# Kernel tuning notes

Hardware: AMD Instinct MI355X
Metric: run time of the kernel (lower is better)

## Reference

```python
import jax, jax.numpy as jnp
import numpy as np

NUM_HEADS = 12


def setup_inputs() -> dict:
    key = jax.random.key(0)
    k0, k1, k2 = jax.random.split(key, 3)
    B, S, D = 2, 2048, 1536
    scale = 1.0 / np.sqrt(D)
    return {
        "hidden_states": jax.random.normal(k0, (B, S, D), dtype=jnp.float32),
        "W_fc": jax.random.normal(k1, (D, D), dtype=jnp.float32) * scale,
        "b_fc": jnp.zeros((D,), dtype=jnp.float32),
        "W_proj": jax.random.normal(k2, (D, D), dtype=jnp.float32) * scale,
        "b_proj": jnp.zeros((D,), dtype=jnp.float32),
    }


def reference(hidden_states, W_fc, b_fc, W_proj, b_proj):
    B, S, D = hidden_states.shape
    H = NUM_HEADS
    hd = D // H
    # value_states: [B, H, S, hd] (key_states == value_states in the original)
    v = (hidden_states @ W_fc.T + b_fc).reshape(B, S, H, hd).transpose(0, 2, 1, 3)
    # Uniform-weight causal sliding-window attention, window_h = 2^(h+1)-1.
    i = jnp.arange(S)[:, None]          # query pos
    j = jnp.arange(S)[None, :]          # key pos
    w = (2 ** jnp.arange(1, H + 1, dtype=jnp.int32) - 1)[:, None, None]  # [H,1,1]
    mask = (j <= i) & (j >= i - w + 1)                                    # [H,S,S]
    valid_len = jnp.minimum(i + 1, w).astype(v.dtype)                     # [H,S,1]
    attn = jnp.where(mask, 1.0 / valid_len, 0.0)                          # [H,S,S]
    # [H,S,S] x [B,H,S,hd] -> [B,S,H,hd] -> [B,S,D]
    out = jnp.einsum("hqk,bhkd->bqhd", attn, v).reshape(B, S, D)
    attn_weights = jnp.broadcast_to(attn[None], (B, H, S, S))
    return out @ W_proj.T + b_proj, attn_weights
```

## Files before the change

### kernel.cpp

```cpp
#include <hip/hip_runtime.h>
#include <hip/hip_bf16.h>

#define S_LEN   2048
#define DMODEL  1536
#define NBATCH  2
#define NHEADS  12
#define MROWS   (NBATCH * S_LEN)
#define NCHUNK  64

#define NGEMM_BLK  384
#define AWB        640
#define AW_ROWS_PER_B  24576u

#define CVT_BLK    10752
#define WA_BLK     3072

typedef unsigned short u16;
typedef __attribute__((ext_vector_type(8))) short bf16x8;
typedef __attribute__((ext_vector_type(4))) float f32x4;

__device__ __forceinline__ u16 f2bf(float x) {
  unsigned u = __float_as_uint(x);
  u += 0x7fffu + ((u >> 16) & 1u);
  return (u16)(u >> 16);
}
__device__ __forceinline__ float bf2f(u16 x) {
  return __uint_as_float(((unsigned)x) << 16);
}

__device__ __forceinline__ void aw_band(float* __restrict__ aw, unsigned r0,
                                        unsigned rcnt, unsigned wv, unsigned nwv) {
  const int lane = threadIdx.x & 63;
  for (unsigned r = r0 + wv; r < r0 + rcnt; r += nwv) {
    const int i  = (int)(r & (S_LEN - 1u));
    const int bh = (int)(r >> 11);
    const int h  = bh >= NHEADS ? bh - NHEADS : bh;
    const int w  = (2 << h) - 1;
    const int lo = max(0, i - w + 1);
    const int len = i - lo + 1;
    const float inv = 1.0f / (float)len;
    float* p = aw + ((size_t)bh << 22) + ((size_t)i << 11) + lo;

    const int mis  = (int)(((size_t)p >> 2) & 3u);
    const int head = min(len, (4 - mis) & 3);
    if (lane < head) p[lane] = inv;
    const int rem = len - head;
    float* pb = p + head;
    const int nv = rem >> 2;
    const f32x4 rv = {inv, inv, inv, inv};
    for (int k = lane; k < nv; k += 64)
      __builtin_nontemporal_store(rv, &((f32x4*)pb)[k]);
    const int tail = rem & 3;
    if (lane < tail) pb[(nv << 2) + lane] = inv;
  }
}

#define N4_HID  1572864
#define N4_W    589824
__global__ void cvt_all(const float4* __restrict__ h, const float4* __restrict__ wf,
                        const float4* __restrict__ wp, ushort4* __restrict__ ho,
                        ushort4* __restrict__ wfo, ushort4* __restrict__ wpo) {
  int t = blockIdx.x * blockDim.x + threadIdx.x;
  const float4* src;
  ushort4* dst;
  int idx;
  if (t < N4_HID)            { src = h;  dst = ho;  idx = t; }
  else if (t < N4_HID + N4_W){ src = wf; dst = wfo; idx = t - N4_HID; }
  else                       { src = wp; dst = wpo; idx = t - N4_HID - N4_W; }
  float4 f = src[idx];
  ushort4 o;
  o.x = f2bf(f.x); o.y = f2bf(f.y); o.z = f2bf(f.z); o.w = f2bf(f.w);
  dst[idx] = o;
}

__device__ __forceinline__ void gld_lds16(u16* lds, const u16* g) {
  __builtin_amdgcn_global_load_lds(
      (const __attribute__((address_space(1))) unsigned int*)g,
      (__attribute__((address_space(3))) unsigned int*)lds, 16, 0, 0);
}

template <bool WITH_CSUM, typename CT>
__global__ __launch_bounds__(256)
void gemm_aw(const u16* __restrict__ A, const u16* __restrict__ B,
             const float* __restrict__ bias, CT* __restrict__ C,
             float* __restrict__ cs, float* __restrict__ aw,
             unsigned row0, int Ndim, int Kdim) {
  if ((int)blockIdx.x >= NGEMM_BLK) {
    const unsigned wv = (blockIdx.x - NGEMM_BLK) * 4u + ((threadIdx.x >> 6) & 3u);
    aw_band(aw, row0, AW_ROWS_PER_B, wv, AWB * 4u);
    return;
  }

  __shared__ __align__(16) u16 As[2][128 * 32];
  __shared__ __align__(16) u16 Bs[2][128 * 32];
  __shared__ float colpart[4][128];

  const int tid  = threadIdx.x;
  const int wave = tid >> 6;
  const int lane = tid & 63;
  const int l15  = lane & 15;
  const int quad = lane >> 4;
  const int bm = (blockIdx.x / (DMODEL / 128)) * 128;
  const int bn = (blockIdx.x % (DMODEL / 128)) * 128;
  const int wm = (wave >> 1) * 64;
  const int wn = (wave & 1) * 64;

  f32x4 acc[4][4] = {};

  const int srow = wave * 32 + (lane >> 2);
  const int skk  = (lane & 3) * 8;
  const u16* gA = A + (size_t)(bm + srow) * Kdim + skk;
  const u16* gB = B + (size_t)(bn + srow) * Kdim + skk;
  u16* lA = (u16*)&As[0][(wave * 32) * 32] - (size_t)0;
  const int lofs = (wave * 32) * 32;
  const size_t rstep16 = (size_t)16 * Kdim;

  gld_lds16(&As[0][lofs],           gA);
  gld_lds16(&As[0][lofs + 16 * 32], gA + rstep16);
  gld_lds16(&Bs[0][lofs],           gB);
  gld_lds16(&Bs[0][lofs + 16 * 32], gB + rstep16);

  int cur = 0;
  for (int k0 = 0; k0 < Kdim; k0 += 32) {
    __syncthreads();
    if (k0 + 32 < Kdim) {
      const int nxt = cur ^ 1;
      gld_lds16(&As[nxt][lofs],           gA + k0 + 32);
      gld_lds16(&As[nxt][lofs + 16 * 32], gA + k0 + 32 + rstep16);
      gld_lds16(&Bs[nxt][lofs],           gB + k0 + 32);
      gld_lds16(&Bs[nxt][lofs + 16 * 32], gB + k0 + 32 + rstep16);
    }

    bf16x8 af[4], bfr[4];
#pragma unroll
    for (int i = 0; i < 4; ++i)
      af[i] = *(const bf16x8*)&As[cur][(wm + i * 16 + l15) * 32 + quad * 8];
#pragma unroll
    for (int j = 0; j < 4; ++j)
      bfr[j] = *(const bf16x8*)&Bs[cur][(wn + j * 16 + l15) * 32 + quad * 8];
#pragma unroll
    for (int i = 0; i < 4; ++i)
#pragma unroll
      for (int j = 0; j < 4; ++j)
        acc[i][j] = __builtin_amdgcn_mfma_f32_16x16x32_bf16(af[i], bfr[j], acc[i][j], 0, 0, 0);
    cur ^= 1;
  }

  const int r0 = quad * 4;
#pragma unroll
  for (int j = 0; j < 4; ++j) {
    const int col = bn + wn + j * 16 + l15;
    const float bj = bias[col];
    float sA = 0.f, sB = 0.f;
#pragma unroll
    for (int i = 0; i < 4; ++i) {
      const int row = bm + wm + i * 16 + r0;
#pragma unroll
      for (int r = 0; r < 4; ++r) {
        float cv = acc[i][j][r] + bj;
        if constexpr (sizeof(CT) == 2) {
          C[(size_t)(row + r) * Ndim + col] = (CT)f2bf(cv);
        } else {
          __builtin_nontemporal_store((CT)cv, &C[(size_t)(row + r) * Ndim + col]);
        }
        if (WITH_CSUM) { if (i < 2) sA += cv; else sB += cv; }
      }
    }
    if (WITH_CSUM) {
      sA += __shfl_xor(sA, 16); sA += __shfl_xor(sA, 32);
      sB += __shfl_xor(sB, 16); sB += __shfl_xor(sB, 32);
      if (quad == 0) {
        colpart[(wm >> 5) | 0][wn + j * 16 + l15] = sA;
        colpart[(wm >> 5) | 1][wn + j * 16 + l15] = sB;
      }
    }
  }
  if (WITH_CSUM) {
    __syncthreads();
    if (tid < 128) {
      const int b  = bm >> 11;
      const int c0 = (bm & 2047) >> 5;
#pragma unroll
      for (int g = 0; g < 4; ++g)
        cs[((size_t)b * NCHUNK + c0 + g) * DMODEL + bn + tid] = colpart[g][tid];
    }
  }
}

__global__ void winavg(const u16* __restrict__ v, const float* __restrict__ cs,
                       u16* __restrict__ A2) {
  int t = blockIdx.x * blockDim.x + threadIdx.x;
  int d = t % DMODEL;
  int s = (t / DMODEL) & 255;
  int b = t / (DMODEL * 256);
  const int h = d >> 7;
  const int w = (2 << h) - 1;
  const u16* vb  = v + (size_t)b * S_LEN * DMODEL + d;
  const float* cb = cs + (size_t)b * NCHUNK * DMODEL + d;

  const int i0 = s * 8;
  const int clead = i0 >> 5;

  int jf = 0, ct = 0;
  const bool ht = (i0 + 7 >= w);
  if (ht) { jf = max(i0, w) - w; ct = jf > 0 ? (jf - 1) >> 5 : 0; }

  float lead = 0.f, tb = 0.f;
  for (int cc = 0; cc < clead; ++cc) {
    float x = cb[(size_t)cc * DMODEL];
    lead += x;
    if (cc < ct) tb += x;
  }
  for (int r = clead * 32; r < i0; ++r)
    lead += bf2f(vb[(size_t)r * DMODEL]);

  float trail = 0.f;
  if (ht && jf > 0) {
    trail = tb;
    for (int r = ct * 32; r < jf; ++r)
      trail += bf2f(vb[(size_t)r * DMODEL]);
  }

  u16* out = A2 + ((size_t)(b * S_LEN + i0)) * DMODEL + d;
#pragma unroll
  for (int rr = 0; rr < 8; ++rr) {
    const int i = i0 + rr;
    lead += bf2f(vb[(size_t)i * DMODEL]);
    float o;
    if (i < w) {
      o = lead / (float)(i + 1);
    } else {
      trail += bf2f(vb[(size_t)(i - w) * DMODEL]);
      o = (lead - trail) / (float)w;
    }
    out[(size_t)rr * DMODEL] = f2bf(o);
  }
}

extern "C" void kernel_launch(void* const* d_in, const int* in_sizes, int n_in,
                              void* d_out, int out_size, void* d_ws, size_t ws_size,
                              hipStream_t stream) {
  const float* hidden = (const float*)d_in[0];
  const float* W_fc   = (const float*)d_in[1];
  const float* b_fc   = (const float*)d_in[2];
  const float* W_proj = (const float*)d_in[3];
  const float* b_proj = (const float*)d_in[4];
  float* outp = (float*)d_out;
  float* aw = outp + (size_t)MROWS * DMODEL;

  char* ws = (char*)d_ws;
  u16*   A16   = (u16*)(ws);
  u16*   Wfc16 = (u16*)(ws + 12582912);
  u16*   Wpj16 = (u16*)(ws + 17301504);
  u16*   v16   = (u16*)(ws + 22020096);
  float* csums = (float*)(ws + 34603008);

  cvt_all<<<CVT_BLK, 256, 0, stream>>>((const float4*)hidden, (const float4*)W_fc,
                                       (const float4*)W_proj, (ushort4*)A16,
                                       (ushort4*)Wfc16, (ushort4*)Wpj16);

  gemm_aw<true, u16><<<NGEMM_BLK + AWB, 256, 0, stream>>>(
      A16, Wfc16, b_fc, v16, csums, aw, 0u, DMODEL, DMODEL);

  winavg<<<WA_BLK, 256, 0, stream>>>(v16, csums, A16);

  gemm_aw<false, float><<<NGEMM_BLK + AWB, 256, 0, stream>>>(
      A16, Wpj16, b_proj, outp, nullptr, aw, AW_ROWS_PER_B, DMODEL, DMODEL);
}
```

Baseline: 519.0 us.

## Fuse fp32-to-bf16 conversion into first GEMM and rebalance attention-weight fill

Removes the standalone conversion kernel. The first GEMM now loads fp32 hidden states and W_fc straight from global memory, converts them to bf16 in registers and stores them to LDS through a register-staged double buffer. W_proj conversion and half of the attention-weight band fill ride along as extra blocks in the first GEMM. The other half of the band fill moves into the window-average kernel, so the second GEMM runs alone. This saves one launch plus a full bf16 round trip of the activations, but the first GEMM now reads twice the bytes and gives up the async global-to-LDS loads.

```diff
diff --git a/kernel.cpp b/kernel.cpp
--- a/kernel.cpp
+++ b/kernel.cpp
@@ -9,11 +9,16 @@
 #define NCHUNK  64
 
 #define NGEMM_BLK  384
-#define AWB        640
+#define WCVT_BLK   256
+#define BAND1_BLK  384
+#define G1_GRID    (NGEMM_BLK + WCVT_BLK + BAND1_BLK)
+
+#define WA_BLK     3072
+#define BAND2_BLK  512
+#define WA_GRID    (WA_BLK + BAND2_BLK)
+
 #define AW_ROWS_PER_B  24576u
-
-#define CVT_BLK    10752
-#define WA_BLK     3072
+#define N4_W    589824u
 
 typedef unsigned short u16;
 typedef __attribute__((ext_vector_type(8))) short bf16x8;
@@ -26,6 +31,10 @@
 }
 __device__ __forceinline__ float bf2f(u16 x) {
   return __uint_as_float(((unsigned)x) << 16);
+}
+__device__ __forceinline__ u16 cvt1(float x) {
+  __hip_bfloat16 h = __float2bfloat16(x);
+  return *(u16*)&h;
 }
 
 __device__ __forceinline__ void aw_band(float* __restrict__ aw, unsigned r0,
@@ -55,45 +64,203 @@
   }
 }
 
-#define N4_HID  1572864
-#define N4_W    589824
-__global__ void cvt_all(const float4* __restrict__ h, const float4* __restrict__ wf,
-                        const float4* __restrict__ wp, ushort4* __restrict__ ho,
-                        ushort4* __restrict__ wfo, ushort4* __restrict__ wpo) {
-  int t = blockIdx.x * blockDim.x + threadIdx.x;
-  const float4* src;
-  ushort4* dst;
-  int idx;
-  if (t < N4_HID)            { src = h;  dst = ho;  idx = t; }
-  else if (t < N4_HID + N4_W){ src = wf; dst = wfo; idx = t - N4_HID; }
-  else                       { src = wp; dst = wpo; idx = t - N4_HID - N4_W; }
-  float4 f = src[idx];
-  ushort4 o;
-  o.x = f2bf(f.x); o.y = f2bf(f.y); o.z = f2bf(f.z); o.w = f2bf(f.w);
-  dst[idx] = o;
-}
-
 __device__ __forceinline__ void gld_lds16(u16* lds, const u16* g) {
   __builtin_amdgcn_global_load_lds(
       (const __attribute__((address_space(1))) unsigned int*)g,
       (__attribute__((address_space(3))) unsigned int*)lds, 16, 0, 0);
 }
 
-template <bool WITH_CSUM, typename CT>
+__device__ __forceinline__ void st8(u16* dst, float4 lo, float4 hi) {
+  ushort4 p0 = { cvt1(lo.x), cvt1(lo.y), cvt1(lo.z), cvt1(lo.w) };
+  ushort4 p1 = { cvt1(hi.x), cvt1(hi.y), cvt1(hi.z), cvt1(hi.w) };
+  *((ushort4*)dst)       = p0;
+  *((ushort4*)(dst + 4)) = p1;
+}
+
 __global__ __launch_bounds__(256)
-void gemm_aw(const u16* __restrict__ A, const u16* __restrict__ B,
-             const float* __restrict__ bias, CT* __restrict__ C,
-             float* __restrict__ cs, float* __restrict__ aw,
-             unsigned row0, int Ndim, int Kdim) {
-  if ((int)blockIdx.x >= NGEMM_BLK) {
-    const unsigned wv = (blockIdx.x - NGEMM_BLK) * 4u + ((threadIdx.x >> 6) & 3u);
-    aw_band(aw, row0, AW_ROWS_PER_B, wv, AWB * 4u);
+void gemm1_fused(const float* __restrict__ A, const float* __restrict__ Bsrc,
+                 const float* __restrict__ bias, u16* __restrict__ C,
+                 float* __restrict__ cs, float* __restrict__ aw,
+                 const float4* __restrict__ wp, ushort4* __restrict__ wpo) {
+  const int blk = blockIdx.x;
+  if (blk >= NGEMM_BLK) {
+    if (blk < NGEMM_BLK + WCVT_BLK) {
+      for (unsigned t = (unsigned)(blk - NGEMM_BLK) * 256u + threadIdx.x;
+           t < N4_W; t += WCVT_BLK * 256u) {
+        float4 f = wp[t];
+        ushort4 o = { f2bf(f.x), f2bf(f.y), f2bf(f.z), f2bf(f.w) };
+        wpo[t] = o;
+      }
+    } else {
+      const unsigned wv = (unsigned)(blk - NGEMM_BLK - WCVT_BLK) * 4u +
+                          ((threadIdx.x >> 6) & 3u);
+      aw_band(aw, 0u, AW_ROWS_PER_B, wv, BAND1_BLK * 4u);
+    }
     return;
   }
 
   __shared__ __align__(16) u16 As[2][128 * 32];
   __shared__ __align__(16) u16 Bs[2][128 * 32];
   __shared__ float colpart[4][128];
+
+  const int tid  = threadIdx.x;
+  const int wave = tid >> 6;
+  const int lane = tid & 63;
+  const int l15  = lane & 15;
+  const int quad = lane >> 4;
+  const int bm = (blk / (DMODEL / 128)) * 128;
+  const int bn = (blk % (DMODEL / 128)) * 128;
+  const int wm = (wave >> 1) * 64;
+  const int wn = (wave & 1) * 64;
+
+  f32x4 acc[4][4] = {};
+
+  const int srow = wave * 32 + (lane >> 2);
+  const int skk  = (lane & 3) * 8;
+  const float* gA = A    + (size_t)(bm + srow) * DMODEL + skk;
+  const float* gB = Bsrc + (size_t)(bn + srow) * DMODEL + skk;
+  const size_t rs16 = (size_t)16 * DMODEL;
+
+  float4 ra0, ra1, ra2, ra3, rb0, rb1, rb2, rb3;
+#define LOADF(k0)                                                        \
+  do {                                                                   \
+    ra0 = *(const float4*)(gA + (k0));                                   \
+    ra1 = *(const float4*)(gA + (k0) + 4);                               \
+    ra2 = *(const float4*)(gA + rs16 + (k0));                            \
+    ra3 = *(const float4*)(gA + rs16 + (k0) + 4);                        \
+    rb0 = *(const float4*)(gB + (k0));                                   \
+    rb1 = *(const float4*)(gB + (k0) + 4);                               \
+    rb2 = *(const float4*)(gB + rs16 + (k0));                            \
+    rb3 = *(const float4*)(gB + rs16 + (k0) + 4);                        \
+  } while (0)
+#define STOREF(buf)                                                      \
+  do {                                                                   \
+    st8(&As[buf][srow * 32 + skk],        ra0, ra1);                     \
+    st8(&As[buf][(srow + 16) * 32 + skk], ra2, ra3);                     \
+    st8(&Bs[buf][srow * 32 + skk],        rb0, rb1);                     \
+    st8(&Bs[buf][(srow + 16) * 32 + skk], rb2, rb3);                     \
+  } while (0)
+
+  LOADF(0);
+  STOREF(0);
+
+  int cur = 0;
+  for (int k0 = 0; k0 < DMODEL; k0 += 32) {
+    __syncthreads();
+    if (k0 + 32 < DMODEL) LOADF(k0 + 32);
+
+    bf16x8 af[4], bfr[4];
+#pragma unroll
+    for (int i = 0; i < 4; ++i)
+      af[i] = *(const bf16x8*)&As[cur][(wm + i * 16 + l15) * 32 + quad * 8];
+#pragma unroll
+    for (int j = 0; j < 4; ++j)
+      bfr[j] = *(const bf16x8*)&Bs[cur][(wn + j * 16 + l15) * 32 + quad * 8];
+#pragma unroll
+    for (int i = 0; i < 4; ++i)
+#pragma unroll
+      for (int j = 0; j < 4; ++j)
+        acc[i][j] = __builtin_amdgcn_mfma_f32_16x16x32_bf16(af[i], bfr[j], acc[i][j], 0, 0, 0);
+
+    if (k0 + 32 < DMODEL) STOREF(cur ^ 1);
+    cur ^= 1;
+  }
+#undef LOADF
+#undef STOREF
+
+  const int r0 = quad * 4;
+#pragma unroll
+  for (int j = 0; j < 4; ++j) {
+    const int col = bn + wn + j * 16 + l15;
+    const float bj = bias[col];
+    float sA = 0.f, sB = 0.f;
+#pragma unroll
+    for (int i = 0; i < 4; ++i) {
+      const int row = bm + wm + i * 16 + r0;
+#pragma unroll
+      for (int r = 0; r < 4; ++r) {
+        float cv = acc[i][j][r] + bj;
+        C[(size_t)(row + r) * DMODEL + col] = f2bf(cv);
+        if (i < 2) sA += cv; else sB += cv;
+      }
+    }
+    sA += __shfl_xor(sA, 16); sA += __shfl_xor(sA, 32);
+    sB += __shfl_xor(sB, 16); sB += __shfl_xor(sB, 32);
+    if (quad == 0) {
+      colpart[(wm >> 5) | 0][wn + j * 16 + l15] = sA;
+      colpart[(wm >> 5) | 1][wn + j * 16 + l15] = sB;
+    }
+  }
+  __syncthreads();
+  if (tid < 128) {
+    const int b  = bm >> 11;
+    const int c0 = (bm & 2047) >> 5;
+#pragma unroll
+    for (int g = 0; g < 4; ++g)
+      cs[((size_t)b * NCHUNK + c0 + g) * DMODEL + bn + tid] = colpart[g][tid];
+  }
+}
+
+__global__ void winavg_aw(const u16* __restrict__ v, const float* __restrict__ cs,
+                          u16* __restrict__ A2, float* __restrict__ aw) {
+  if ((int)blockIdx.x >= WA_BLK) {
+    const unsigned wv = (blockIdx.x - WA_BLK) * 4u + ((threadIdx.x >> 6) & 3u);
+    aw_band(aw, AW_ROWS_PER_B, AW_ROWS_PER_B, wv, BAND2_BLK * 4u);
+    return;
+  }
+  int t = blockIdx.x * blockDim.x + threadIdx.x;
+  int d = t % DMODEL;
+  int s = (t / DMODEL) & 255;
+  int b = t / (DMODEL * 256);
+  const int h = d >> 7;
+  const int w = (2 << h) - 1;
+  const u16* vb  = v + (size_t)b * S_LEN * DMODEL + d;
+  const float* cb = cs + (size_t)b * NCHUNK * DMODEL + d;
+
+  const int i0 = s * 8;
+  const int clead = i0 >> 5;
+
+  int jf = 0, ct = 0;
+  const bool ht = (i0 + 7 >= w);
+  if (ht) { jf = max(i0, w) - w; ct = jf > 0 ? (jf - 1) >> 5 : 0; }
+
+  float lead = 0.f, tb = 0.f;
+  for (int cc = 0; cc < clead; ++cc) {
+    float x = cb[(size_t)cc * DMODEL];
+    lead += x;
+    if (cc < ct) tb += x;
+  }
+  for (int r = clead * 32; r < i0; ++r)
+    lead += bf2f(vb[(size_t)r * DMODEL]);
+
+  float trail = 0.f;
+  if (ht && jf > 0) {
+    trail = tb;
+    for (int r = ct * 32; r < jf; ++r)
+      trail += bf2f(vb[(size_t)r * DMODEL]);
+  }
+
+  u16* out = A2 + ((size_t)(b * S_LEN + i0)) * DMODEL + d;
+#pragma unroll
+  for (int rr = 0; rr < 8; ++rr) {
+    const int i = i0 + rr;
+    lead += bf2f(vb[(size_t)i * DMODEL]);
+    float o;
+    if (i < w) {
+      o = lead / (float)(i + 1);
+    } else {
+      trail += bf2f(vb[(size_t)(i - w) * DMODEL]);
+      o = (lead - trail) / (float)w;
+    }
+    out[(size_t)rr * DMODEL] = f2bf(o);
+  }
+}
+
+__global__ __launch_bounds__(256)
+void gemm2(const u16* __restrict__ A, const u16* __restrict__ B,
+           const float* __restrict__ bias, float* __restrict__ C) {
+  __shared__ __align__(16) u16 As[2][128 * 32];
+  __shared__ __align__(16) u16 Bs[2][128 * 32];
 
   const int tid  = threadIdx.x;
   const int wave = tid >> 6;
@@ -109,11 +276,10 @@
 
   const int srow = wave * 32 + (lane >> 2);
   const int skk  = (lane & 3) * 8;
-  const u16* gA = A + (size_t)(bm + srow) * Kdim + skk;
-  const u16* gB = B + (size_t)(bn + srow) * Kdim + skk;
-  u16* lA = (u16*)&As[0][(wave * 32) * 32] - (size_t)0;
+  const u16* gA = A + (size_t)(bm + srow) * DMODEL + skk;
+  const u16* gB = B + (size_t)(bn + srow) * DMODEL + skk;
   const int lofs = (wave * 32) * 32;
-  const size_t rstep16 = (size_t)16 * Kdim;
+  const size_t rstep16 = (size_t)16 * DMODEL;
 
   gld_lds16(&As[0][lofs],           gA);
   gld_lds16(&As[0][lofs + 16 * 32], gA + rstep16);
@@ -121,9 +287,9 @@
   gld_lds16(&Bs[0][lofs + 16 * 32], gB + rstep16);
 
   int cur = 0;
-  for (int k0 = 0; k0 < Kdim; k0 += 32) {
+  for (int k0 = 0; k0 < DMODEL; k0 += 32) {
     __syncthreads();
-    if (k0 + 32 < Kdim) {
+    if (k0 + 32 < DMODEL) {
       const int nxt = cur ^ 1;
       gld_lds16(&As[nxt][lofs],           gA + k0 + 32);
       gld_lds16(&As[nxt][lofs + 16 * 32], gA + k0 + 32 + rstep16);
@@ -151,89 +317,15 @@
   for (int j = 0; j < 4; ++j) {
     const int col = bn + wn + j * 16 + l15;
     const float bj = bias[col];
-    float sA = 0.f, sB = 0.f;
 #pragma unroll
     for (int i = 0; i < 4; ++i) {
       const int row = bm + wm + i * 16 + r0;
 #pragma unroll
       for (int r = 0; r < 4; ++r) {
-        float cv = acc[i][j][r] + bj;
-        if constexpr (sizeof(CT) == 2) {
-          C[(size_t)(row + r) * Ndim + col] = (CT)f2bf(cv);
-        } else {
-          __builtin_nontemporal_store((CT)cv, &C[(size_t)(row + r) * Ndim + col]);
-        }
-        if (WITH_CSUM) { if (i < 2) sA += cv; else sB += cv; }
+        __builtin_nontemporal_store(acc[i][j][r] + bj,
+                                    &C[(size_t)(row + r) * DMODEL + col]);
       }
     }
-    if (WITH_CSUM) {
-      sA += __shfl_xor(sA, 16); sA += __shfl_xor(sA, 32);
-      sB += __shfl_xor(sB, 16); sB += __shfl_xor(sB, 32);
-      if (quad == 0) {
-        colpart[(wm >> 5) | 0][wn + j * 16 + l15] = sA;
-        colpart[(wm >> 5) | 1][wn + j * 16 + l15] = sB;
-      }
-    }
-  }
-  if (WITH_CSUM) {
-    __syncthreads();
-    if (tid < 128) {
-      const int b  = bm >> 11;
-      const int c0 = (bm & 2047) >> 5;
-#pragma unroll
-      for (int g = 0; g < 4; ++g)
-        cs[((size_t)b * NCHUNK + c0 + g) * DMODEL + bn + tid] = colpart[g][tid];
-    }
-  }
-}
-
-__global__ void winavg(const u16* __restrict__ v, const float* __restrict__ cs,
-                       u16* __restrict__ A2) {
-  int t = blockIdx.x * blockDim.x + threadIdx.x;
-  int d = t % DMODEL;
-  int s = (t / DMODEL) & 255;
-  int b = t / (DMODEL * 256);
-  const int h = d >> 7;
-  const int w = (2 << h) - 1;
-  const u16* vb  = v + (size_t)b * S_LEN * DMODEL + d;
-  const float* cb = cs + (size_t)b * NCHUNK * DMODEL + d;
-
-  const int i0 = s * 8;
-  const int clead = i0 >> 5;
-
-  int jf = 0, ct = 0;
-  const bool ht = (i0 + 7 >= w);
-  if (ht) { jf = max(i0, w) - w; ct = jf > 0 ? (jf - 1) >> 5 : 0; }
-
-  float lead = 0.f, tb = 0.f;
-  for (int cc = 0; cc < clead; ++cc) {
-    float x = cb[(size_t)cc * DMODEL];
-    lead += x;
-    if (cc < ct) tb += x;
-  }
-  for (int r = clead * 32; r < i0; ++r)
-    lead += bf2f(vb[(size_t)r * DMODEL]);
-
-  float trail = 0.f;
-  if (ht && jf > 0) {
-    trail = tb;
-    for (int r = ct * 32; r < jf; ++r)
-      trail += bf2f(vb[(size_t)r * DMODEL]);
-  }
-
-  u16* out = A2 + ((size_t)(b * S_LEN + i0)) * DMODEL + d;
-#pragma unroll
-  for (int rr = 0; rr < 8; ++rr) {
-    const int i = i0 + rr;
-    lead += bf2f(vb[(size_t)i * DMODEL]);
-    float o;
-    if (i < w) {
-      o = lead / (float)(i + 1);
-    } else {
-      trail += bf2f(vb[(size_t)(i - w) * DMODEL]);
-      o = (lead - trail) / (float)w;
-    }
-    out[(size_t)rr * DMODEL] = f2bf(o);
   }
 }
 
@@ -250,20 +342,14 @@
 
   char* ws = (char*)d_ws;
   u16*   A16   = (u16*)(ws);
-  u16*   Wfc16 = (u16*)(ws + 12582912);
   u16*   Wpj16 = (u16*)(ws + 17301504);
   u16*   v16   = (u16*)(ws + 22020096);
   float* csums = (float*)(ws + 34603008);
 
-  cvt_all<<<CVT_BLK, 256, 0, stream>>>((const float4*)hidden, (const float4*)W_fc,
-                                       (const float4*)W_proj, (ushort4*)A16,
-                                       (ushort4*)Wfc16, (ushort4*)Wpj16);
-
-  gemm_aw<true, u16><<<NGEMM_BLK + AWB, 256, 0, stream>>>(
-      A16, Wfc16, b_fc, v16, csums, aw, 0u, DMODEL, DMODEL);
-
-  winavg<<<WA_BLK, 256, 0, stream>>>(v16, csums, A16);
-
-  gemm_aw<false, float><<<NGEMM_BLK + AWB, 256, 0, stream>>>(
-      A16, Wpj16, b_proj, outp, nullptr, aw, AW_ROWS_PER_B, DMODEL, DMODEL);
-}
+  gemm1_fused<<<G1_GRID, 256, 0, stream>>>(
+      hidden, W_fc, b_fc, v16, csums, aw, (const float4*)W_proj, (ushort4*)Wpj16);
+
+  winavg_aw<<<WA_GRID, 256, 0, stream>>>(v16, csums, A16, aw);
+
+  gemm2<<<NGEMM_BLK, 256, 0, stream>>>(A16, Wpj16, b_proj, outp);
+}
```

Measured after the change: 532.5 us. 2.6% more time.

## Fuse conversion, GEMMs, window average and mask writes into one persistent kernel

Applied to the files above, without the earlier changes.

Replaces the four separate launches with a single persistent kernel of 768 blocks that runs conversion, first GEMM plus attention-weight band, window averaging, and second GEMM plus band. The phases are separated by atomic-counter grid barriers whose counters are zeroed by a memset each call. This removes launch gaps and inter-kernel drain. The window-average stage now handles 32 rows per thread using chunk sums directly, cutting redundant prefix reads. In exchange it adds barrier spin costs, gives fewer blocks to the bandwidth-heavy mask writes, and relies on all blocks being co-resident.

```diff
diff --git a/kernel.cpp b/kernel.cpp
--- a/kernel.cpp
+++ b/kernel.cpp
@@ -8,12 +8,22 @@
 #define MROWS   (NBATCH * S_LEN)
 #define NCHUNK  64
 
-#define NGEMM_BLK  384
-#define AWB        640
+#define GRID    768
+#define NTHR    256
+#define GEMMB   384
+#define BANDB   (GRID - GEMMB)
+
 #define AW_ROWS_PER_B  24576u
-
-#define CVT_BLK    10752
-#define WA_BLK     3072
+#define N4_HID  1572864u
+#define N4_W    589824u
+#define N4_ALL  2752512u
+
+#define WS_A16    0u
+#define WS_WFC    12582912u
+#define WS_WPJ    17301504u
+#define WS_V16    22020096u
+#define WS_CSUM   34603008u
+#define WS_CTR    35389440u
 
 typedef unsigned short u16;
 typedef __attribute__((ext_vector_type(8))) short bf16x8;
@@ -26,6 +36,23 @@
 }
 __device__ __forceinline__ float bf2f(u16 x) {
   return __uint_as_float(((unsigned)x) << 16);
+}
+__device__ __forceinline__ void gld_lds16(u16* lds, const u16* g) {
+  __builtin_amdgcn_global_load_lds(
+      (const __attribute__((address_space(1))) unsigned int*)g,
+      (__attribute__((address_space(3))) unsigned int*)lds, 16, 0, 0);
+}
+
+__device__ __forceinline__ void grid_barrier(unsigned* cnt) {
+  __syncthreads();
+  if (threadIdx.x == 0) {
+    __threadfence();
+    __hip_atomic_fetch_add(cnt, 1u, __ATOMIC_ACQ_REL, __HIP_MEMORY_SCOPE_AGENT);
+    while (__hip_atomic_load(cnt, __ATOMIC_ACQUIRE, __HIP_MEMORY_SCOPE_AGENT) < GRID)
+      __builtin_amdgcn_s_sleep(1);
+    __threadfence();
+  }
+  __syncthreads();
 }
 
 __device__ __forceinline__ void aw_band(float* __restrict__ aw, unsigned r0,
@@ -55,53 +82,18 @@
   }
 }
 
-#define N4_HID  1572864
-#define N4_W    589824
-__global__ void cvt_all(const float4* __restrict__ h, const float4* __restrict__ wf,
-                        const float4* __restrict__ wp, ushort4* __restrict__ ho,
-                        ushort4* __restrict__ wfo, ushort4* __restrict__ wpo) {
-  int t = blockIdx.x * blockDim.x + threadIdx.x;
-  const float4* src;
-  ushort4* dst;
-  int idx;
-  if (t < N4_HID)            { src = h;  dst = ho;  idx = t; }
-  else if (t < N4_HID + N4_W){ src = wf; dst = wfo; idx = t - N4_HID; }
-  else                       { src = wp; dst = wpo; idx = t - N4_HID - N4_W; }
-  float4 f = src[idx];
-  ushort4 o;
-  o.x = f2bf(f.x); o.y = f2bf(f.y); o.z = f2bf(f.z); o.w = f2bf(f.w);
-  dst[idx] = o;
-}
-
-__device__ __forceinline__ void gld_lds16(u16* lds, const u16* g) {
-  __builtin_amdgcn_global_load_lds(
-      (const __attribute__((address_space(1))) unsigned int*)g,
-      (__attribute__((address_space(3))) unsigned int*)lds, 16, 0, 0);
-}
-
 template <bool WITH_CSUM, typename CT>
-__global__ __launch_bounds__(256)
-void gemm_aw(const u16* __restrict__ A, const u16* __restrict__ B,
-             const float* __restrict__ bias, CT* __restrict__ C,
-             float* __restrict__ cs, float* __restrict__ aw,
-             unsigned row0, int Ndim, int Kdim) {
-  if ((int)blockIdx.x >= NGEMM_BLK) {
-    const unsigned wv = (blockIdx.x - NGEMM_BLK) * 4u + ((threadIdx.x >> 6) & 3u);
-    aw_band(aw, row0, AW_ROWS_PER_B, wv, AWB * 4u);
-    return;
-  }
-
-  __shared__ __align__(16) u16 As[2][128 * 32];
-  __shared__ __align__(16) u16 Bs[2][128 * 32];
-  __shared__ float colpart[4][128];
-
+__device__ __forceinline__ void gemm_tile(
+    const u16* __restrict__ A, const u16* __restrict__ B,
+    const float* __restrict__ bias, CT* __restrict__ C, float* __restrict__ cs,
+    int blk, u16 (*As)[128 * 32], u16 (*Bs)[128 * 32], float (*colpart)[128]) {
   const int tid  = threadIdx.x;
   const int wave = tid >> 6;
   const int lane = tid & 63;
   const int l15  = lane & 15;
   const int quad = lane >> 4;
-  const int bm = (blockIdx.x / (DMODEL / 128)) * 128;
-  const int bn = (blockIdx.x % (DMODEL / 128)) * 128;
+  const int bm = (blk / (DMODEL / 128)) * 128;
+  const int bn = (blk % (DMODEL / 128)) * 128;
   const int wm = (wave >> 1) * 64;
   const int wn = (wave & 1) * 64;
 
@@ -109,11 +101,10 @@
 
   const int srow = wave * 32 + (lane >> 2);
   const int skk  = (lane & 3) * 8;
-  const u16* gA = A + (size_t)(bm + srow) * Kdim + skk;
-  const u16* gB = B + (size_t)(bn + srow) * Kdim + skk;
-  u16* lA = (u16*)&As[0][(wave * 32) * 32] - (size_t)0;
+  const u16* gA = A + (size_t)(bm + srow) * DMODEL + skk;
+  const u16* gB = B + (size_t)(bn + srow) * DMODEL + skk;
   const int lofs = (wave * 32) * 32;
-  const size_t rstep16 = (size_t)16 * Kdim;
+  const size_t rstep16 = (size_t)16 * DMODEL;
 
   gld_lds16(&As[0][lofs],           gA);
   gld_lds16(&As[0][lofs + 16 * 32], gA + rstep16);
@@ -121,9 +112,9 @@
   gld_lds16(&Bs[0][lofs + 16 * 32], gB + rstep16);
 
   int cur = 0;
-  for (int k0 = 0; k0 < Kdim; k0 += 32) {
+  for (int k0 = 0; k0 < DMODEL; k0 += 32) {
     __syncthreads();
-    if (k0 + 32 < Kdim) {
+    if (k0 + 32 < DMODEL) {
       const int nxt = cur ^ 1;
       gld_lds16(&As[nxt][lofs],           gA + k0 + 32);
       gld_lds16(&As[nxt][lofs + 16 * 32], gA + k0 + 32 + rstep16);
@@ -159,9 +150,9 @@
       for (int r = 0; r < 4; ++r) {
         float cv = acc[i][j][r] + bj;
         if constexpr (sizeof(CT) == 2) {
-          C[(size_t)(row + r) * Ndim + col] = (CT)f2bf(cv);
+          C[(size_t)(row + r) * DMODEL + col] = (CT)f2bf(cv);
         } else {
-          __builtin_nontemporal_store((CT)cv, &C[(size_t)(row + r) * Ndim + col]);
+          __builtin_nontemporal_store((CT)cv, &C[(size_t)(row + r) * DMODEL + col]);
         }
         if (WITH_CSUM) { if (i < 2) sA += cv; else sB += cv; }
       }
@@ -187,33 +178,29 @@
   }
 }
 
-__global__ void winavg(const u16* __restrict__ v, const float* __restrict__ cs,
-                       u16* __restrict__ A2) {
-  int t = blockIdx.x * blockDim.x + threadIdx.x;
-  int d = t % DMODEL;
-  int s = (t / DMODEL) & 255;
-  int b = t / (DMODEL * 256);
+__device__ __forceinline__ void winavg32(unsigned t, const u16* __restrict__ v,
+                                         const float* __restrict__ cs,
+                                         u16* __restrict__ A2) {
+  const int d = (int)(t % DMODEL);
+  const int s = (int)((t / DMODEL) & 63);
+  const int b = (int)(t / (DMODEL * 64));
   const int h = d >> 7;
   const int w = (2 << h) - 1;
   const u16* vb  = v + (size_t)b * S_LEN * DMODEL + d;
   const float* cb = cs + (size_t)b * NCHUNK * DMODEL + d;
 
-  const int i0 = s * 8;
-  const int clead = i0 >> 5;
+  const int i0 = s * 32;
 
   int jf = 0, ct = 0;
-  const bool ht = (i0 + 7 >= w);
+  const bool ht = (i0 + 31 >= w);
   if (ht) { jf = max(i0, w) - w; ct = jf > 0 ? (jf - 1) >> 5 : 0; }
 
   float lead = 0.f, tb = 0.f;
-  for (int cc = 0; cc < clead; ++cc) {
+  for (int cc = 0; cc < s; ++cc) {
     float x = cb[(size_t)cc * DMODEL];
     lead += x;
     if (cc < ct) tb += x;
   }
-  for (int r = clead * 32; r < i0; ++r)
-    lead += bf2f(vb[(size_t)r * DMODEL]);
-
   float trail = 0.f;
   if (ht && jf > 0) {
     trail = tb;
@@ -222,8 +209,8 @@
   }
 
   u16* out = A2 + ((size_t)(b * S_LEN + i0)) * DMODEL + d;
-#pragma unroll
-  for (int rr = 0; rr < 8; ++rr) {
+#pragma unroll 8
+  for (int rr = 0; rr < 32; ++rr) {
     const int i = i0 + rr;
     lead += bf2f(vb[(size_t)i * DMODEL]);
     float o;
@@ -237,33 +224,66 @@
   }
 }
 
+__global__ __launch_bounds__(NTHR, 3) void mega(
+    const float4* __restrict__ hid, const float4* __restrict__ wf,
+    const float4* __restrict__ wp, const float* __restrict__ b_fc,
+    const float* __restrict__ b_proj, float* __restrict__ outp,
+    char* __restrict__ ws) {
+  __shared__ __align__(16) u16 As[2][128 * 32];
+  __shared__ __align__(16) u16 Bs[2][128 * 32];
+  __shared__ float colpart[4][128];
+
+  u16*   A16   = (u16*)(ws + WS_A16);
+  u16*   Wfc16 = (u16*)(ws + WS_WFC);
+  u16*   Wpj16 = (u16*)(ws + WS_WPJ);
+  u16*   v16   = (u16*)(ws + WS_V16);
+  float* csums = (float*)(ws + WS_CSUM);
+  unsigned* ctr = (unsigned*)(ws + WS_CTR);
+  float* aw    = outp + (size_t)MROWS * DMODEL;
+
+  const unsigned blk = blockIdx.x;
+  const unsigned gstride = GRID * NTHR;
+
+  for (unsigned t = blk * NTHR + threadIdx.x; t < N4_ALL; t += gstride) {
+    const float4* src; ushort4* dst; unsigned idx;
+    if (t < N4_HID)             { src = hid; dst = (ushort4*)A16;   idx = t; }
+    else if (t < N4_HID + N4_W) { src = wf;  dst = (ushort4*)Wfc16; idx = t - N4_HID; }
+    else                        { src = wp;  dst = (ushort4*)Wpj16; idx = t - N4_HID - N4_W; }
+    float4 f = src[idx];
+    ushort4 o = { f2bf(f.x), f2bf(f.y), f2bf(f.z), f2bf(f.w) };
+    dst[idx] = o;
+  }
+  grid_barrier(&ctr[0]);
+
+  if (blk < GEMMB)
+    gemm_tile<true, u16>(A16, Wfc16, b_fc, v16, csums, (int)blk, As, Bs, colpart);
+  else
+    aw_band(aw, 0u, AW_ROWS_PER_B,
+            (blk - GEMMB) * 4u + ((threadIdx.x >> 6) & 3u), BANDB * 4u);
+  grid_barrier(&ctr[4]);
+
+  winavg32(blk * NTHR + threadIdx.x, v16, csums, A16);
+  grid_barrier(&ctr[8]);
+
+  if (blk < GEMMB)
+    gemm_tile<false, float>(A16, Wpj16, b_proj, outp, nullptr, (int)blk, As, Bs, colpart);
+  else
+    aw_band(aw, AW_ROWS_PER_B, AW_ROWS_PER_B,
+            (blk - GEMMB) * 4u + ((threadIdx.x >> 6) & 3u), BANDB * 4u);
+}
+
 extern "C" void kernel_launch(void* const* d_in, const int* in_sizes, int n_in,
                               void* d_out, int out_size, void* d_ws, size_t ws_size,
                               hipStream_t stream) {
-  const float* hidden = (const float*)d_in[0];
-  const float* W_fc   = (const float*)d_in[1];
-  const float* b_fc   = (const float*)d_in[2];
-  const float* W_proj = (const float*)d_in[3];
-  const float* b_proj = (const float*)d_in[4];
+  const float4* hid = (const float4*)d_in[0];
+  const float4* wf  = (const float4*)d_in[1];
+  const float*  bfc = (const float*)d_in[2];
+  const float4* wp  = (const float4*)d_in[3];
+  const float*  bpj = (const float*)d_in[4];
   float* outp = (float*)d_out;
-  float* aw = outp + (size_t)MROWS * DMODEL;
-
-  char* ws = (char*)d_ws;
-  u16*   A16   = (u16*)(ws);
-  u16*   Wfc16 = (u16*)(ws + 12582912);
-  u16*   Wpj16 = (u16*)(ws + 17301504);
-  u16*   v16   = (u16*)(ws + 22020096);
-  float* csums = (float*)(ws + 34603008);
-
-  cvt_all<<<CVT_BLK, 256, 0, stream>>>((const float4*)hidden, (const float4*)W_fc,
-                                       (const float4*)W_proj, (ushort4*)A16,
-                                       (ushort4*)Wfc16, (ushort4*)Wpj16);
-
-  gemm_aw<true, u16><<<NGEMM_BLK + AWB, 256, 0, stream>>>(
-      A16, Wfc16, b_fc, v16, csums, aw, 0u, DMODEL, DMODEL);
-
-  winavg<<<WA_BLK, 256, 0, stream>>>(v16, csums, A16);
-
-  gemm_aw<false, float><<<NGEMM_BLK + AWB, 256, 0, stream>>>(
-      A16, Wpj16, b_proj, outp, nullptr, aw, AW_ROWS_PER_B, DMODEL, DMODEL);
-}
+  char*  ws   = (char*)d_ws;
+
+  hipMemsetAsync(ws + WS_CTR, 0, 64, stream);
+
+  mega<<<GRID, NTHR, 0, stream>>>(hid, wf, wp, bfc, bpj, outp, ws);
+}
```

Result: slower. 1.363 ms (+162.5%).
